# Optimization experiments

Measured on AMD Instinct MI355X. Metric: run time of the kernel, lower is better.

Reference implementation:

```python
import jax, jax.numpy as jnp
import numpy as np

B = 100000
D = 32          # per-modality feature dim
SCALE = 1.0 / jnp.sqrt(2.0 * D)  # 1/sqrt(64)


def setup_inputs() -> dict:
    key = jax.random.key(0)
    k1, k2, k3, k4 = jax.random.split(key, 4)
    return {
        "f1_norm": jax.random.normal(k1, (B, D), dtype=jnp.float32),
        "f2_norm": jax.random.normal(k2, (B, D), dtype=jnp.float32),
        "W_ca": jax.random.normal(k3, (1, 2 * D), dtype=jnp.float32) * 0.1,
        "W_cv": jax.random.normal(k4, (1, 2 * D), dtype=jnp.float32) * 0.1,
    }


def reference(f1_norm, f2_norm, W_ca, W_cv):
    # av: concat of audio and visual feats, [B, 64]
    av = jnp.concatenate([f1_norm, f2_norm], axis=-1)
    # per-sample outer-product attention: aud_fts^T @ aud_vis_fts -> [B, 32, 64]
    audio_att = jnp.tanh(f1_norm[:, :, None] * av[:, None, :] * SCALE)
    vis_att = jnp.tanh(f2_norm[:, :, None] * av[:, None, :] * SCALE)
    # Linear(64,1,no bias): contract last dim with weight row -> [B, 32]
    H_a = 0.1 * jax.nn.relu(jnp.einsum('bij,j->bi', audio_att, W_ca[0]) + f1_norm)
    H_v = 0.1 * jax.nn.relu(jnp.einsum('bij,j->bi', vis_att, W_cv[0]) + f2_norm)
    # concat H_a^T, H_v^T per sample -> [B, 1, 64]
    return jnp.concatenate([H_a, H_v], axis=-1)[:, None, :]
```

## Files before the change

kernel.cpp:

```cpp
#include <hip/hip_runtime.h>


__global__ __launch_bounds__(256) void cam_kernel(
    const float* __restrict__ f1,
    const float* __restrict__ f2,
    const float* __restrict__ Wca,
    const float* __restrict__ Wcv,
    float* __restrict__ out,
    int B)
{
    constexpr float C = 0.3606737602222409f;

    __shared__ float s_w2d[2][128];
    __shared__ float s_wsum[2];
    __shared__ __align__(16) float s_avd[4][128];

    const int tid  = threadIdx.x;
    const int lane = tid & 63;
    const int wid  = tid >> 6;

    {
        const int r = tid >> 7;
        const int c = tid & 127;
        const float w = (r ? Wcv : Wca)[c & 63];
        s_w2d[r][c] = -2.0f * w;
    }
    if (tid < 128) {
        const int r = wid;
        float s = (r ? Wcv : Wca)[lane];
        #pragma unroll
        for (int off = 32; off > 0; off >>= 1) s += __shfl_xor(s, off, 64);
        if (lane == 0) s_wsum[r] = s;
    }
    __syncthreads();

    const int sel = lane >> 5;
    const float wsum = s_wsum[sel];
    const float* __restrict__ w2base = &s_w2d[sel][lane];
    float* __restrict__ avw = s_avd[wid];
    const float* __restrict__ avbase = &avw[lane];
    const float* __restrict__ fbase = sel ? f2 : f1;
    const int col = lane & 31;
    const int lane4 = lane << 2;

    const int gw     = (blockIdx.x * 256 + tid) >> 6;
    const int stride = (gridDim.x * 256) >> 6;

    int b = gw;
    if (b >= B) return;
    float x = fbase[b * 32 + col];

    while (b < B) {
        const int bn = b + stride;
        float xn = 0.0f;
        if (bn < B) xn = fbase[bn * 32 + col];

        const float xc = x * C;
        avw[lane]      = xc;
        avw[lane + 64] = xc;
        asm volatile("s_waitcnt lgkmcnt(0)" ::: "memory");
        __builtin_amdgcn_sched_barrier(0);

        float accA, accB = 0.0f, accC = 0.0f, accD = 0.0f;
        {
            const float p = __builtin_amdgcn_rcpf(1.0f + __builtin_amdgcn_exp2f(x * xc));
            accA = p * w2base[0];
        }
        int idx = lane4;
        #pragma unroll
        for (int k = 1; k < 32; ++k) {
            idx = (idx - 4) & 252;
            const float a = avbase[k];
            const float p = __builtin_amdgcn_rcpf(1.0f + __builtin_amdgcn_exp2f(x * a));
            if (k & 1) accB = fmaf(p, w2base[k], accB);
            else       accA = fmaf(p, w2base[k], accA);
            const float q = __int_as_float(
                __builtin_amdgcn_ds_bpermute(idx, __float_as_int(p)));
            if (k & 1) accC = fmaf(q, w2base[64 - k], accC);
            else       accD = fmaf(q, w2base[64 - k], accD);
        }
        {
            const float a = avbase[32];
            const float p = __builtin_amdgcn_rcpf(1.0f + __builtin_amdgcn_exp2f(x * a));
            accD = fmaf(p, w2base[32], accD);
        }

        float h = wsum + x + ((accA + accB) + (accC + accD));
        h = fmaxf(h, 0.0f) * 0.1f;
        out[b * 64 + lane] = h;

        b = bn;
        x = xn;
    }
}

extern "C" void kernel_launch(void* const* d_in, const int* in_sizes, int n_in,
                              void* d_out, int out_size, void* d_ws, size_t ws_size,
                              hipStream_t stream) {
    const float* f1  = (const float*)d_in[0];
    const float* f2  = (const float*)d_in[1];
    const float* Wca = (const float*)d_in[2];
    const float* Wcv = (const float*)d_in[3];
    float* out = (float*)d_out;

    const int B = in_sizes[0] / 32;
    int blocks = (B + 3) / 4;
    if (blocks > 2048) blocks = 2048;
    if (blocks < 1) blocks = 1;

    cam_kernel<<<blocks, 256, 0, stream>>>(f1, f2, Wca, Wcv, out, B);
}
```

Measured before the change: 148.1 us.

## Replace LDS broadcast and bpermute reduction with DPP row-rotate accumulation

The per-sample inner loop no longer stages scaled features in LDS and uses a bpermute per step for the symmetric term. It now rotates both the operand and a running partial sum across the wave with DPP, and reads pre-permuted weight quads from shared memory as float4. Blocks grow from 256 to 512 threads with a matching grid cap. The intent is to remove LDS store/wait and bpermute latency from the hot loop. In exchange it adds a serial dependency chain through the rotated accumulator and a larger shared weight table.

After: 162.3 us. +9.6%, slower.

```diff
diff --git a/kernel.cpp b/kernel.cpp
--- a/kernel.cpp
+++ b/kernel.cpp
@@ -1,7 +1,12 @@
 #include <hip/hip_runtime.h>
 
 
-__global__ __launch_bounds__(256) void cam_kernel(
+__device__ __forceinline__ float wave_ror1_f32(float v) {
+    return __int_as_float(__builtin_amdgcn_update_dpp(
+        __float_as_int(v), __float_as_int(v), 0x13C, 0xF, 0xF, false));
+}
+
+__global__ __launch_bounds__(512, 8) void cam_kernel(
     const float* __restrict__ f1,
     const float* __restrict__ f2,
     const float* __restrict__ Wca,
@@ -11,40 +16,53 @@
 {
     constexpr float C = 0.3606737602222409f;
 
-    __shared__ float s_w2d[2][128];
+    __shared__ __align__(16) float4 s_P4[2][15][64];
+    __shared__ __align__(8)  float2 s_P1[2][64];
     __shared__ float s_wsum[2];
-    __shared__ __align__(16) float s_avd[4][128];
 
     const int tid  = threadIdx.x;
     const int lane = tid & 63;
-    const int wid  = tid >> 6;
 
-    {
-        const int r = tid >> 7;
-        const int c = tid & 127;
-        const float w = (r ? Wcv : Wca)[c & 63];
-        s_w2d[r][c] = -2.0f * w;
+    for (int idx = tid; idx < 2048; idx += 512) {
+        const int sel = idx >> 10;
+        const int kp  = (idx >> 6) & 15;
+        const int ln  = idx & 63;
+        if (kp < 15) {
+            const int k1 = 31 - 2 * kp, k0 = 30 - 2 * kp;
+            const int j1 = (ln + k1) & 63, j0 = (ln + k0) & 63;
+            const float* Ws = sel ? Wcv : Wca;
+            s_P4[sel][kp][ln] = make_float4(
+                -2.0f * Ws[j1], -2.0f * ((j1 < 32) ? Wca : Wcv)[ln],
+                -2.0f * Ws[j0], -2.0f * ((j0 < 32) ? Wca : Wcv)[ln]);
+        }
     }
     if (tid < 128) {
-        const int r = wid;
-        float s = (r ? Wcv : Wca)[lane];
+        const int sel = tid >> 6;
+        const int j = (lane + 1) & 63;
+        s_P1[sel][lane] = make_float2(
+            -2.0f * (sel ? Wcv : Wca)[j],
+            -2.0f * ((j < 32) ? Wca : Wcv)[lane]);
+        float s = (sel ? Wcv : Wca)[lane];
         #pragma unroll
         for (int off = 32; off > 0; off >>= 1) s += __shfl_xor(s, off, 64);
-        if (lane == 0) s_wsum[r] = s;
+        if (lane == 0) s_wsum[sel] = s;
     }
     __syncthreads();
 
     const int sel = lane >> 5;
     const float wsum = s_wsum[sel];
-    const float* __restrict__ w2base = &s_w2d[sel][lane];
-    float* __restrict__ avw = s_avd[wid];
-    const float* __restrict__ avbase = &avw[lane];
+    const float4* __restrict__ P4p = &s_P4[sel][0][lane];
+    const float2* __restrict__ P1p = &s_P1[sel][lane];
     const float* __restrict__ fbase = sel ? f2 : f1;
     const int col = lane & 31;
-    const int lane4 = lane << 2;
 
-    const int gw     = (blockIdx.x * 256 + tid) >> 6;
-    const int stride = (gridDim.x * 256) >> 6;
+    const float w0  = -2.0f * (sel ? Wcv : Wca)[lane];
+    const float w32 = -2.0f * (sel ? Wcv : Wca)[lane ^ 32];
+    const int idx31 = ((lane + 31) & 63) << 2;
+    const int idx32 = (lane ^ 32) << 2;
+
+    const int gw     = (blockIdx.x * 512 + tid) >> 6;
+    const int stride = gridDim.x << 3;
 
     int b = gw;
     if (b >= B) return;
@@ -56,36 +74,38 @@
         if (bn < B) xn = fbase[bn * 32 + col];
 
         const float xc = x * C;
-        avw[lane]      = xc;
-        avw[lane + 64] = xc;
-        asm volatile("s_waitcnt lgkmcnt(0)" ::: "memory");
-        __builtin_amdgcn_sched_barrier(0);
+        float a = __int_as_float(
+            __builtin_amdgcn_ds_bpermute(idx31, __float_as_int(xc)));
+        const float a32 = __int_as_float(
+            __builtin_amdgcn_ds_bpermute(idx32, __float_as_int(xc)));
 
-        float accA, accB = 0.0f, accC = 0.0f, accD = 0.0f;
-        {
-            const float p = __builtin_amdgcn_rcpf(1.0f + __builtin_amdgcn_exp2f(x * xc));
-            accA = p * w2base[0];
-        }
-        int idx = lane4;
+        float own1 = __builtin_amdgcn_rcpf(1.0f + __builtin_amdgcn_exp2f(x * a32)) * w32;
+        float own0 = __builtin_amdgcn_rcpf(1.0f + __builtin_amdgcn_exp2f(x * xc)) * w0;
+
+        float t = 0.0f;
         #pragma unroll
-        for (int k = 1; k < 32; ++k) {
-            idx = (idx - 4) & 252;
-            const float a = avbase[k];
-            const float p = __builtin_amdgcn_rcpf(1.0f + __builtin_amdgcn_exp2f(x * a));
-            if (k & 1) accB = fmaf(p, w2base[k], accB);
-            else       accA = fmaf(p, w2base[k], accA);
-            const float q = __int_as_float(
-                __builtin_amdgcn_ds_bpermute(idx, __float_as_int(p)));
-            if (k & 1) accC = fmaf(q, w2base[64 - k], accC);
-            else       accD = fmaf(q, w2base[64 - k], accD);
+        for (int kp = 0; kp < 15; ++kp) {
+            const float4 w4 = P4p[kp * 64];
+            float p = __builtin_amdgcn_rcpf(1.0f + __builtin_amdgcn_exp2f(x * a));
+            own0 = fmaf(p, w4.x, own0);
+            t = fmaf(p, w4.y, t);
+            t = wave_ror1_f32(t);
+            a = wave_ror1_f32(a);
+            p = __builtin_amdgcn_rcpf(1.0f + __builtin_amdgcn_exp2f(x * a));
+            own1 = fmaf(p, w4.z, own1);
+            t = fmaf(p, w4.w, t);
+            t = wave_ror1_f32(t);
+            a = wave_ror1_f32(a);
         }
         {
-            const float a = avbase[32];
+            const float2 w2 = P1p[0];
             const float p = __builtin_amdgcn_rcpf(1.0f + __builtin_amdgcn_exp2f(x * a));
-            accD = fmaf(p, w2base[32], accD);
+            own0 = fmaf(p, w2.x, own0);
+            t = fmaf(p, w2.y, t);
+            t = wave_ror1_f32(t);
         }
 
-        float h = wsum + x + ((accA + accB) + (accC + accD));
+        float h = wsum + x + own0 + own1 + t;
         h = fmaxf(h, 0.0f) * 0.1f;
         out[b * 64 + lane] = h;
 
@@ -104,9 +124,9 @@
     float* out = (float*)d_out;
 
     const int B = in_sizes[0] / 32;
-    int blocks = (B + 3) / 4;
-    if (blocks > 2048) blocks = 2048;
+    int blocks = (B + 7) / 8;
+    if (blocks > 1024) blocks = 1024;
     if (blocks < 1) blocks = 1;
 
-    cam_kernel<<<blocks, 256, 0, stream>>>(f1, f2, Wca, Wcv, out, B);
+    cam_kernel<<<blocks, 512, 0, stream>>>(f1, f2, Wca, Wcv, out, B);
 }
```
